# Performance work log

Hardware: AMD Instinct MI355X
Metric: run time of the kernel (lower is better)

Reference implementation:

```python
import jax, jax.numpy as jnp
import numpy as np

N_NODES = 100000
N_EDGES = 1600000
D = 128            # in_channels == hidden_channels
N_CLASSES = 10
N_GRAPHS = 512
N_CONVS = 3        # num_layers - 1


def _linear_params(key, d_in, d_out):
    kw, kb = jax.random.split(key)
    bound = 1.0 / np.sqrt(d_in)
    w = jax.random.uniform(kw, (d_in, d_out), jnp.float32, -bound, bound)
    b = jax.random.uniform(kb, (d_out,), jnp.float32, -bound, bound)
    return w, b


def setup_inputs() -> dict:
    key = jax.random.key(0)
    ks = jax.random.split(key, 16)
    x = jax.random.normal(ks[0], (N_NODES, D), jnp.float32)
    edge_index = jax.random.randint(ks[1], (2, N_EDGES), 0, N_NODES, jnp.int64)
    batch = jnp.sort(jax.random.randint(ks[2], (N_NODES,), 0, N_GRAPHS, jnp.int64))
    inp = {"x": x, "edge_index": edge_index, "batch": batch}
    # 3 GIN convs, each an MLP: Linear(D,D) -> ReLU -> Linear(D,D)
    for i in range(N_CONVS):
        w1, b1 = _linear_params(ks[3 + 2 * i], D, D)
        w2, b2 = _linear_params(ks[4 + 2 * i], D, D)
        inp[f"w1_{i}"], inp[f"b1_{i}"] = w1, b1
        inp[f"w2_{i}"], inp[f"b2_{i}"] = w2, b2
    wl, bl = _linear_params(ks[10], D, N_CLASSES)
    inp["w_lin"], inp["b_lin"] = wl, bl
    return inp


def _gin_conv(x, src, dst, w1, b1, w2, b2):
    # sum_{j->i} x_j  (scatter-add over edges), eps = 0 (PyG default)
    agg = jax.ops.segment_sum(x[src], dst, num_segments=N_NODES)
    h = agg + x  # (1 + eps) * x + aggregate
    h = jax.nn.relu(h @ w1 + b1) @ w2 + b2  # nn.Sequential MLP
    return h


def reference(x, edge_index, batch,
              w1_0, b1_0, w2_0, b2_0,
              w1_1, b1_1, w2_1, b2_1,
              w1_2, b1_2, w2_2, b2_2,
              w_lin, b_lin):
    src, dst = edge_index[0], edge_index[1]
    params = [(w1_0, b1_0, w2_0, b2_0),
              (w1_1, b1_1, w2_1, b2_1),
              (w1_2, b1_2, w2_2, b2_2)]
    for (w1, b1, w2, b2) in params:
        x = _gin_conv(x, src, dst, w1, b1, w2, b2)
        x = jax.nn.relu(x)
    pooled = jax.ops.segment_sum(x, batch, num_segments=N_GRAPHS)  # global_add_pool
    return pooled @ w_lin + b_lin
```

## Files before the change

kernel.cpp:

```cpp
#include <hip/hip_runtime.h>
#include <hip/hip_bf16.h>

#define N_NODES 100000
#define N_EDGES 1600000
#define DIM 128
#define N_GRAPHS 512
#define N_CLASSES 10
#define SCAN_CHUNK 1024

#define NBK 782
#define EB 8192
#define NEB 196
#define HN (NBK * NEB)
#define NCH_HIST ((HN + SCAN_CHUNK - 1) / SCAN_CHUNK)
#define NCH_CNT ((N_NODES + SCAN_CHUNK - 1) / SCAN_CHUNK)

#define POOL_CHUNK 128
#define NPB ((N_NODES + POOL_CHUNK - 1) / POOL_CHUNK)

typedef __attribute__((ext_vector_type(8))) short short8;
typedef __attribute__((ext_vector_type(4))) float floatx4;

__device__ __forceinline__ uint bfround(float f) {
    uint u = __builtin_bit_cast(uint, f);
    return (u + 0x7fffu + ((u >> 16) & 1u)) >> 16;
}
__device__ __forceinline__ float bflo(uint u) { return __builtin_bit_cast(float, u << 16); }
__device__ __forceinline__ float bfhi(uint u) { return __builtin_bit_cast(float, u & 0xffff0000u); }
__device__ __forceinline__ float bf2f(ushort u) { return __builtin_bit_cast(float, (uint)u << 16); }

__device__ __forceinline__ void addrow(float* a, uint4 v) {
    a[0] += bflo(v.x); a[1] += bfhi(v.x);
    a[2] += bflo(v.y); a[3] += bfhi(v.y);
    a[4] += bflo(v.z); a[5] += bfhi(v.z);
    a[6] += bflo(v.w); a[7] += bfhi(v.w);
}


__global__ void k_cvt_x(const float* __restrict__ x, ushort* __restrict__ xb, int n4) {
    int i = blockIdx.x * blockDim.x + threadIdx.x;
    int stride = gridDim.x * blockDim.x;
    for (; i < n4; i += stride) {
        floatx4 v = *(const floatx4*)(x + (size_t)i * 4);
        ushort4 o;
        o.x = (ushort)bfround(v.x);
        o.y = (ushort)bfround(v.y);
        o.z = (ushort)bfround(v.z);
        o.w = (ushort)bfround(v.w);
        *(ushort4*)(xb + (size_t)i * 4) = o;
    }
}

struct WPtrs { const float* w[6]; };

__global__ __launch_bounds__(256) void k_cvt_w(WPtrs wp, ushort* __restrict__ Wt) {
    int m = blockIdx.x >> 6;
    int idx = (blockIdx.x & 63) * 256 + threadIdx.x;
    int n = idx >> 7, k = idx & 127;
    Wt[(size_t)m * 16384 + idx] = (ushort)bfround(wp.w[m][k * 128 + n]);
}


__global__ void k_zero(int* __restrict__ p, int n) {
    int i = blockIdx.x * blockDim.x + threadIdx.x;
    int stride = gridDim.x * blockDim.x;
    for (; i < n; i += stride) p[i] = 0;
}

__global__ __launch_bounds__(256) void k_hist(const int* __restrict__ dstv,
                                              int* __restrict__ hist) {
    __shared__ int cnt[NBK];
    int blk = blockIdx.x, tid = threadIdx.x;
    for (int i = tid; i < NBK; i += 256) cnt[i] = 0;
    __syncthreads();
    int base = blk * EB;
    int end = min(base + EB, N_EDGES);
    for (int i = base + tid; i < end; i += 256) atomicAdd(&cnt[dstv[i] >> 7], 1);
    __syncthreads();
    for (int b = tid; b < NBK; b += 256) hist[b * NEB + blk] = cnt[b];
}

__global__ __launch_bounds__(256) void k_reduce(const int* __restrict__ src, int n,
                                                int* __restrict__ chunk_sums) {
    int base = blockIdx.x * SCAN_CHUNK;
    int tid = threadIdx.x;
    int s = 0;
    for (int i = tid; i < SCAN_CHUNK; i += 256) {
        int idx = base + i;
        if (idx < n) s += src[idx];
    }
    __shared__ int red[256];
    red[tid] = s;
    __syncthreads();
    for (int off = 128; off > 0; off >>= 1) {
        if (tid < off) red[tid] += red[tid + off];
        __syncthreads();
    }
    if (tid == 0) chunk_sums[blockIdx.x] = red[0];
}

__global__ __launch_bounds__(256) void k_scan_c(int* __restrict__ chunk_sums, int nch,
                                                int* __restrict__ total_out) {
    __shared__ int sm[256];
    int tid = threadIdx.x;
    int v = (tid < nch) ? chunk_sums[tid] : 0;
    sm[tid] = v;
    __syncthreads();
    for (int off = 1; off < 256; off <<= 1) {
        int t = (tid >= off) ? sm[tid - off] : 0;
        __syncthreads();
        sm[tid] += t;
        __syncthreads();
    }
    if (tid < nch) chunk_sums[tid] = sm[tid] - v;
    if (tid == 255) *total_out = sm[255];
}

__global__ __launch_bounds__(256) void k_apply(const int* __restrict__ src,
                                               const int* __restrict__ chunk_sums,
                                               int* __restrict__ dst, int n) {
    int base = blockIdx.x * SCAN_CHUNK;
    int tid = threadIdx.x;
    int i0 = base + tid * 4;
    int v[4];
    int s = 0;
    #pragma unroll
    for (int j = 0; j < 4; j++) {
        int idx = i0 + j;
        v[j] = (idx < n) ? src[idx] : 0;
        s += v[j];
    }
    __shared__ int sc[256];
    sc[tid] = s;
    __syncthreads();
    for (int off = 1; off < 256; off <<= 1) {
        int t = (tid >= off) ? sc[tid - off] : 0;
        __syncthreads();
        sc[tid] += t;
        __syncthreads();
    }
    int excl = sc[tid] - s + chunk_sums[blockIdx.x];
    #pragma unroll
    for (int j = 0; j < 4; j++) {
        int idx = i0 + j;
        if (idx < n) dst[idx] = excl;
        excl += v[j];
    }
}

__global__ __launch_bounds__(256) void k_scatter(const int* __restrict__ srcv,
                                                 const int* __restrict__ dstv,
                                                 const int* __restrict__ hists,
                                                 uint* __restrict__ sorted) {
    __shared__ int cur[NBK];
    int blk = blockIdx.x, tid = threadIdx.x;
    for (int b = tid; b < NBK; b += 256) cur[b] = hists[b * NEB + blk];
    __syncthreads();
    int base = blk * EB;
    int end = min(base + EB, N_EDGES);
    for (int i = base + tid; i < end; i += 256) {
        int s = srcv[i], d = dstv[i];
        int p = atomicAdd(&cur[d >> 7], 1);
        sorted[p] = (uint)s | ((uint)(d & 127) << 17);
    }
}

__global__ __launch_bounds__(256) void k_bcount_s(const int* __restrict__ hists,
                                                  const uint* __restrict__ sorted,
                                                  int* __restrict__ counts) {
    __shared__ int cnt[128];
    int b = blockIdx.x, tid = threadIdx.x;
    if (tid < 128) cnt[tid] = 0;
    __syncthreads();
    int s0 = hists[b * NEB];
    int s1 = (b == NBK - 1) ? N_EDGES : hists[(b + 1) * NEB];
    for (int i = s0 + tid; i < s1; i += 256) atomicAdd(&cnt[(sorted[i] >> 17) & 127], 1);
    __syncthreads();
    int node = (b << 7) + tid;
    if (tid < 128 && node < N_NODES) counts[node] = cnt[tid];
}

__global__ __launch_bounds__(256) void k_fill_s(const int* __restrict__ hists,
                                                const uint* __restrict__ sorted,
                                                const int* __restrict__ row_ptr,
                                                int* __restrict__ col) {
    __shared__ int cur[128];
    int b = blockIdx.x, tid = threadIdx.x;
    int node = (b << 7) + tid;
    if (tid < 128 && node < N_NODES) cur[tid] = row_ptr[node];
    __syncthreads();
    int s0 = hists[b * NEB];
    int s1 = (b == NBK - 1) ? N_EDGES : hists[(b + 1) * NEB];
    for (int i = s0 + tid; i < s1; i += 256) {
        uint e = sorted[i];
        int p = atomicAdd(&cur[(e >> 17) & 127], 1);
        col[p] = (int)(e & 0x1FFFFu);
    }
}

__global__ __launch_bounds__(256) void k_agg(const uint4* __restrict__ xr,
                                             const int* __restrict__ row_ptr,
                                             const int* __restrict__ col,
                                             uint4* __restrict__ hr) {
    int node = (blockIdx.x << 2) + (threadIdx.x >> 6);
    if (node >= N_NODES) return;
    int lane = threadIdx.x & 63;
    int grp = lane >> 4;
    int l16 = lane & 15;

    float acc[8];
    if (grp == 0) {
        uint4 sv = xr[(size_t)node * 16 + l16];
        acc[0] = bflo(sv.x); acc[1] = bfhi(sv.x);
        acc[2] = bflo(sv.y); acc[3] = bfhi(sv.y);
        acc[4] = bflo(sv.z); acc[5] = bfhi(sv.z);
        acc[6] = bflo(sv.w); acc[7] = bfhi(sv.w);
    } else {
        #pragma unroll
        for (int i = 0; i < 8; i++) acc[i] = 0.f;
    }

    int b = row_ptr[node], e = row_ptr[node + 1];
    for (int j0 = b; j0 < e; j0 += 64) {
        int rem = e - j0;
        int chunk = rem < 64 ? rem : 64;
        int myidx = (lane < chunk) ? col[j0 + lane] : 0;
        int iters = (chunk + 15) >> 4;
        for (int f = 0; f < iters; f++) {
            int p = (f << 4) + grp;
            int s0 = __shfl(myidx, (p      < chunk) ? p      : 0);
            int s1 = __shfl(myidx, (p + 4  < chunk) ? p + 4  : 0);
            int s2 = __shfl(myidx, (p + 8  < chunk) ? p + 8  : 0);
            int s3 = __shfl(myidx, (p + 12 < chunk) ? p + 12 : 0);
            uint4 v0 = xr[(size_t)s0 * 16 + l16];
            uint4 v1 = xr[(size_t)s1 * 16 + l16];
            uint4 v2 = xr[(size_t)s2 * 16 + l16];
            uint4 v3 = xr[(size_t)s3 * 16 + l16];
            if (p < chunk)      addrow(acc, v0);
            if (p + 4 < chunk)  addrow(acc, v1);
            if (p + 8 < chunk)  addrow(acc, v2);
            if (p + 12 < chunk) addrow(acc, v3);
        }
    }

    #pragma unroll
    for (int i = 0; i < 8; i++) {
        acc[i] += __shfl_xor(acc[i], 16);
        acc[i] += __shfl_xor(acc[i], 32);
    }

    if (grp == 0) {
        uint4 o;
        o.x = bfround(acc[0]) | (bfround(acc[1]) << 16);
        o.y = bfround(acc[2]) | (bfround(acc[3]) << 16);
        o.z = bfround(acc[4]) | (bfround(acc[5]) << 16);
        o.w = bfround(acc[6]) | (bfround(acc[7]) << 16);
        hr[(size_t)node * 16 + l16] = o;
    }
}

__device__ __forceinline__ int loff(int row, int byte) {
    return row * 256 + (byte ^ ((row & 7) << 4));
}

__global__ __launch_bounds__(256) void k_mlp(const ushort* __restrict__ hin,
                                             ushort* __restrict__ xout,
                                             const ushort* __restrict__ W1t,
                                             const float* __restrict__ b1,
                                             const ushort* __restrict__ W2t,
                                             const float* __restrict__ b2) {
    __shared__ alignas(16) char hT[64 * 256];
    __shared__ alignas(16) char tT[64 * 256];
    int tid = threadIdx.x;
    int lane = tid & 63;
    int wave = tid >> 6;
    int node0 = blockIdx.x * 64;
    int l15 = lane & 15;
    int lhi = lane >> 4;

    #pragma unroll
    for (int it = 0; it < 4; ++it) {
        int idx = it * 256 + tid;
        int row = idx >> 4;
        int cb = (idx & 15) * 16;
        int gn = node0 + row;
        floatx4 v = {0.f, 0.f, 0.f, 0.f};
        if (gn < N_NODES) v = *(const floatx4*)(hin + (size_t)gn * 128 + cb / 2);
        *(floatx4*)(hT + loff(row, cb)) = v;
    }
    __syncthreads();

    int ncol0 = wave * 32;
    short8 bf[4][2];
    #pragma unroll
    for (int ks = 0; ks < 4; ks++)
        #pragma unroll
        for (int nf = 0; nf < 2; nf++) {
            int nrow = ncol0 + nf * 16 + l15;
            bf[ks][nf] = *(const short8*)(W1t + nrow * 128 + ks * 32 + lhi * 8);
        }

    floatx4 acc[4][2];
    #pragma unroll
    for (int m = 0; m < 4; m++)
        #pragma unroll
        for (int nf = 0; nf < 2; nf++) {
            float bias = b1[ncol0 + nf * 16 + l15];
            acc[m][nf] = (floatx4){bias, bias, bias, bias};
        }

    #pragma unroll
    for (int ks = 0; ks < 4; ks++) {
        short8 af[4];
        #pragma unroll
        for (int m = 0; m < 4; m++)
            af[m] = *(const short8*)(hT + loff(m * 16 + l15, ks * 64 + lhi * 16));
        #pragma unroll
        for (int m = 0; m < 4; m++)
            #pragma unroll
            for (int nf = 0; nf < 2; nf++)
                acc[m][nf] = __builtin_amdgcn_mfma_f32_16x16x32_bf16(af[m], bf[ks][nf], acc[m][nf], 0, 0, 0);
    }
    #pragma unroll
    for (int m = 0; m < 4; m++)
        #pragma unroll
        for (int nf = 0; nf < 2; nf++) {
            int colb = (ncol0 + nf * 16 + l15) * 2;
            #pragma unroll
            for (int j = 0; j < 4; j++) {
                int row = m * 16 + lhi * 4 + j;
                float t = acc[m][nf][j];
                t = t > 0.f ? t : 0.f;
                *(ushort*)(tT + loff(row, colb)) = (ushort)bfround(t);
            }
        }
    __syncthreads();

    #pragma unroll
    for (int ks = 0; ks < 4; ks++)
        #pragma unroll
        for (int nf = 0; nf < 2; nf++) {
            int nrow = ncol0 + nf * 16 + l15;
            bf[ks][nf] = *(const short8*)(W2t + nrow * 128 + ks * 32 + lhi * 8);
        }
    #pragma unroll
    for (int m = 0; m < 4; m++)
        #pragma unroll
        for (int nf = 0; nf < 2; nf++) {
            float bias = b2[ncol0 + nf * 16 + l15];
            acc[m][nf] = (floatx4){bias, bias, bias, bias};
        }

    #pragma unroll
    for (int ks = 0; ks < 4; ks++) {
        short8 af[4];
        #pragma unroll
        for (int m = 0; m < 4; m++)
            af[m] = *(const short8*)(tT + loff(m * 16 + l15, ks * 64 + lhi * 16));
        #pragma unroll
        for (int m = 0; m < 4; m++)
            #pragma unroll
            for (int nf = 0; nf < 2; nf++)
                acc[m][nf] = __builtin_amdgcn_mfma_f32_16x16x32_bf16(af[m], bf[ks][nf], acc[m][nf], 0, 0, 0);
    }
    #pragma unroll
    for (int m = 0; m < 4; m++)
        #pragma unroll
        for (int nf = 0; nf < 2; nf++) {
            int colb = (ncol0 + nf * 16 + l15) * 2;
            #pragma unroll
            for (int j = 0; j < 4; j++) {
                int row = m * 16 + lhi * 4 + j;
                float t = acc[m][nf][j];
                t = t > 0.f ? t : 0.f;
                *(ushort*)(hT + loff(row, colb)) = (ushort)bfround(t);
            }
        }
    __syncthreads();
    #pragma unroll
    for (int it = 0; it < 4; ++it) {
        int idx = it * 256 + tid;
        int row = idx >> 4;
        int cb = (idx & 15) * 16;
        int gn = node0 + row;
        if (gn < N_NODES)
            *(floatx4*)(xout + (size_t)gn * 128 + cb / 2) = *(const floatx4*)(hT + loff(row, cb));
    }
}

__global__ __launch_bounds__(256) void k_pool(const uint* __restrict__ x,
                                              const int* __restrict__ batch,
                                              float* __restrict__ pooled) {
    int n0 = blockIdx.x * POOL_CHUNK;
    int wave = threadIdx.x >> 6;
    int lane = threadIdx.x & 63;
    float a0 = 0.f, a1 = 0.f;
    int cur = -1;
    int endn = min(n0 + POOL_CHUNK, N_NODES);
    for (int n = n0 + wave; n < endn; n += 4) {
        int g = batch[n];
        if (g != cur) {
            if (cur >= 0) {
                atomicAdd(&pooled[cur * 128 + lane * 2], a0);
                atomicAdd(&pooled[cur * 128 + lane * 2 + 1], a1);
            }
            cur = g; a0 = 0.f; a1 = 0.f;
        }
        uint v = x[(size_t)n * 64 + lane];
        a0 += bflo(v); a1 += bfhi(v);
    }
    if (cur >= 0) {
        atomicAdd(&pooled[cur * 128 + lane * 2], a0);
        atomicAdd(&pooled[cur * 128 + lane * 2 + 1], a1);
    }
}

__global__ __launch_bounds__(64) void k_final(const float* __restrict__ pooled,
                                              const float* __restrict__ wl,
                                              const float* __restrict__ bl,
                                              float* __restrict__ out) {
    int g = blockIdx.x;
    int o = threadIdx.x;
    if (o >= N_CLASSES) return;
    float acc = bl[o];
    for (int k = 0; k < 128; k++) acc += pooled[g * 128 + k] * wl[k * N_CLASSES + o];
    out[g * N_CLASSES + o] = acc;
}


extern "C" void kernel_launch(void* const* d_in, const int* in_sizes, int n_in,
                              void* d_out, int out_size, void* d_ws, size_t ws_size,
                              hipStream_t stream) {
    const float* x0  = (const float*)d_in[0];
    const int* ei    = (const int*)d_in[1];
    const int* batch = (const int*)d_in[2];
    const float* W1[3] = {(const float*)d_in[3], (const float*)d_in[7],  (const float*)d_in[11]};
    const float* B1[3] = {(const float*)d_in[4], (const float*)d_in[8],  (const float*)d_in[12]};
    const float* W2[3] = {(const float*)d_in[5], (const float*)d_in[9],  (const float*)d_in[13]};
    const float* B2[3] = {(const float*)d_in[6], (const float*)d_in[10], (const float*)d_in[14]};
    const float* wl = (const float*)d_in[15];
    const float* bl = (const float*)d_in[16];
    float* out = (float*)d_out;

    const int* srcv = ei;
    const int* dstv = ei + N_EDGES;

    char* w = (char*)d_ws;
    ushort* xb = (ushort*)w;
    ushort* hb = xb + (size_t)N_NODES * DIM;
    ushort* wt = hb + (size_t)N_NODES * DIM;
    float* pooled = (float*)(wt + 6 * 128 * 128);
    int* row_ptr = (int*)(pooled + N_GRAPHS * DIM);
    int* counts  = row_ptr + (N_NODES + 2);
    int* colidx  = counts + N_NODES;
    int* chunk_sums = colidx + N_EDGES;
    int* hist    = chunk_sums + 256;
    uint* sorted = (uint*)(hist + HN + 1);

    hipLaunchKernelGGL(k_cvt_x, dim3(2048), dim3(256), 0, stream, x0, xb, N_NODES * DIM / 4);
    WPtrs wp;
    wp.w[0] = W1[0]; wp.w[1] = W2[0]; wp.w[2] = W1[1];
    wp.w[3] = W2[1]; wp.w[4] = W1[2]; wp.w[5] = W2[2];
    hipLaunchKernelGGL(k_cvt_w, dim3(6 * 64), dim3(256), 0, stream, wp, wt);
    hipLaunchKernelGGL(k_zero, dim3(64), dim3(256), 0, stream, (int*)pooled, N_GRAPHS * DIM);

    hipLaunchKernelGGL(k_hist, dim3(NEB), dim3(256), 0, stream, dstv, hist);
    hipLaunchKernelGGL(k_reduce, dim3(NCH_HIST), dim3(256), 0, stream, hist, HN, chunk_sums);
    hipLaunchKernelGGL(k_scan_c, dim3(1), dim3(256), 0, stream, chunk_sums, NCH_HIST, hist + HN);
    hipLaunchKernelGGL(k_apply, dim3(NCH_HIST), dim3(256), 0, stream, hist, chunk_sums, hist, HN);
    hipLaunchKernelGGL(k_scatter, dim3(NEB), dim3(256), 0, stream, srcv, dstv, hist, sorted);
    hipLaunchKernelGGL(k_bcount_s, dim3(NBK), dim3(256), 0, stream, hist, sorted, counts);
    hipLaunchKernelGGL(k_reduce, dim3(NCH_CNT), dim3(256), 0, stream, counts, N_NODES, chunk_sums);
    hipLaunchKernelGGL(k_scan_c, dim3(1), dim3(256), 0, stream, chunk_sums, NCH_CNT, row_ptr + N_NODES);
    hipLaunchKernelGGL(k_apply, dim3(NCH_CNT), dim3(256), 0, stream, counts, chunk_sums, row_ptr, N_NODES);
    hipLaunchKernelGGL(k_fill_s, dim3(NBK), dim3(256), 0, stream, hist, sorted, row_ptr, colidx);

    dim3 aggGrid((N_NODES + 3) / 4), aggBlk(256);
    dim3 mlpGrid((N_NODES + 63) / 64), mlpBlk(256);
    for (int l = 0; l < 3; l++) {
        hipLaunchKernelGGL(k_agg, aggGrid, aggBlk, 0, stream,
                           (const uint4*)xb, row_ptr, colidx, (uint4*)hb);
        hipLaunchKernelGGL(k_mlp, mlpGrid, mlpBlk, 0, stream,
                           hb, xb, wt + (size_t)(2 * l) * 16384, B1[l],
                           wt + (size_t)(2 * l + 1) * 16384, B2[l]);
    }

    hipLaunchKernelGGL(k_pool, dim3(NPB), dim3(256), 0, stream, (const uint*)xb, batch, pooled);
    hipLaunchKernelGGL(k_final, dim3(N_GRAPHS), dim3(64), 0, stream, pooled, wl, bl, out);
}
```

Before: 346.3 us.

## Fuse neighbor aggregation into GIN MLP kernel with ping-pong buffers

Merges the separate aggregation and MLP kernels into one kernel. Each block gathers and sums neighbor rows for its 64-node tile straight into swizzled shared memory, then runs the MFMA MLP on that tile. Two ping-pong buffers replace the intermediate bf16 round trip through global memory. This removes one write and one read of the aggregated features per layer, plus one launch. The cost is that each wave now handles 16 nodes in sequence, which gives fewer independent waves to hide gather latency, raises register and LDS pressure per block, and adds load imbalance from skewed degrees.

Result: slower. 380.1 us (+9.7%).

```diff
diff --git a/kernel.cpp b/kernel.cpp
--- a/kernel.cpp
+++ b/kernel.cpp
@@ -18,6 +18,9 @@
 #define POOL_CHUNK 128
 #define NPB ((N_NODES + POOL_CHUNK - 1) / POOL_CHUNK)
 
+#define GIN_TILE 64
+#define NGB ((N_NODES + GIN_TILE - 1) / GIN_TILE)
+
 typedef __attribute__((ext_vector_type(8))) short short8;
 typedef __attribute__((ext_vector_type(4))) float floatx4;
 
@@ -27,7 +30,6 @@
 }
 __device__ __forceinline__ float bflo(uint u) { return __builtin_bit_cast(float, u << 16); }
 __device__ __forceinline__ float bfhi(uint u) { return __builtin_bit_cast(float, u & 0xffff0000u); }
-__device__ __forceinline__ float bf2f(ushort u) { return __builtin_bit_cast(float, (uint)u << 16); }
 
 __device__ __forceinline__ void addrow(float* a, uint4 v) {
     a[0] += bflo(v.x); a[1] += bfhi(v.x);
@@ -198,72 +200,13 @@
     }
 }
 
-__global__ __launch_bounds__(256) void k_agg(const uint4* __restrict__ xr,
+__device__ __forceinline__ int loff(int row, int byte) {
+    return row * 256 + (byte ^ ((row & 7) << 4));
+}
+
+__global__ __launch_bounds__(256) void k_gin(const uint4* __restrict__ xr,
                                              const int* __restrict__ row_ptr,
                                              const int* __restrict__ col,
-                                             uint4* __restrict__ hr) {
-    int node = (blockIdx.x << 2) + (threadIdx.x >> 6);
-    if (node >= N_NODES) return;
-    int lane = threadIdx.x & 63;
-    int grp = lane >> 4;
-    int l16 = lane & 15;
-
-    float acc[8];
-    if (grp == 0) {
-        uint4 sv = xr[(size_t)node * 16 + l16];
-        acc[0] = bflo(sv.x); acc[1] = bfhi(sv.x);
-        acc[2] = bflo(sv.y); acc[3] = bfhi(sv.y);
-        acc[4] = bflo(sv.z); acc[5] = bfhi(sv.z);
-        acc[6] = bflo(sv.w); acc[7] = bfhi(sv.w);
-    } else {
-        #pragma unroll
-        for (int i = 0; i < 8; i++) acc[i] = 0.f;
-    }
-
-    int b = row_ptr[node], e = row_ptr[node + 1];
-    for (int j0 = b; j0 < e; j0 += 64) {
-        int rem = e - j0;
-        int chunk = rem < 64 ? rem : 64;
-        int myidx = (lane < chunk) ? col[j0 + lane] : 0;
-        int iters = (chunk + 15) >> 4;
-        for (int f = 0; f < iters; f++) {
-            int p = (f << 4) + grp;
-            int s0 = __shfl(myidx, (p      < chunk) ? p      : 0);
-            int s1 = __shfl(myidx, (p + 4  < chunk) ? p + 4  : 0);
-            int s2 = __shfl(myidx, (p + 8  < chunk) ? p + 8  : 0);
-            int s3 = __shfl(myidx, (p + 12 < chunk) ? p + 12 : 0);
-            uint4 v0 = xr[(size_t)s0 * 16 + l16];
-            uint4 v1 = xr[(size_t)s1 * 16 + l16];
-            uint4 v2 = xr[(size_t)s2 * 16 + l16];
-            uint4 v3 = xr[(size_t)s3 * 16 + l16];
-            if (p < chunk)      addrow(acc, v0);
-            if (p + 4 < chunk)  addrow(acc, v1);
-            if (p + 8 < chunk)  addrow(acc, v2);
-            if (p + 12 < chunk) addrow(acc, v3);
-        }
-    }
-
-    #pragma unroll
-    for (int i = 0; i < 8; i++) {
-        acc[i] += __shfl_xor(acc[i], 16);
-        acc[i] += __shfl_xor(acc[i], 32);
-    }
-
-    if (grp == 0) {
-        uint4 o;
-        o.x = bfround(acc[0]) | (bfround(acc[1]) << 16);
-        o.y = bfround(acc[2]) | (bfround(acc[3]) << 16);
-        o.z = bfround(acc[4]) | (bfround(acc[5]) << 16);
-        o.w = bfround(acc[6]) | (bfround(acc[7]) << 16);
-        hr[(size_t)node * 16 + l16] = o;
-    }
-}
-
-__device__ __forceinline__ int loff(int row, int byte) {
-    return row * 256 + (byte ^ ((row & 7) << 4));
-}
-
-__global__ __launch_bounds__(256) void k_mlp(const ushort* __restrict__ hin,
                                              ushort* __restrict__ xout,
                                              const ushort* __restrict__ W1t,
                                              const float* __restrict__ b1,
@@ -274,22 +217,71 @@
     int tid = threadIdx.x;
     int lane = tid & 63;
     int wave = tid >> 6;
-    int node0 = blockIdx.x * 64;
+    int node0 = blockIdx.x * GIN_TILE;
+    int grp = lane >> 4;
+    int l16 = lane & 15;
+
+    for (int i = 0; i < 16; i++) {
+        int row = wave * 16 + i;
+        int node = node0 + row;
+        if (node >= N_NODES) {
+            if (grp == 0) *(uint4*)(hT + loff(row, l16 * 16)) = make_uint4(0, 0, 0, 0);
+            continue;
+        }
+        float acc[8];
+        if (grp == 0) {
+            uint4 sv = xr[(size_t)node * 16 + l16];
+            acc[0] = bflo(sv.x); acc[1] = bfhi(sv.x);
+            acc[2] = bflo(sv.y); acc[3] = bfhi(sv.y);
+            acc[4] = bflo(sv.z); acc[5] = bfhi(sv.z);
+            acc[6] = bflo(sv.w); acc[7] = bfhi(sv.w);
+        } else {
+            #pragma unroll
+            for (int q = 0; q < 8; q++) acc[q] = 0.f;
+        }
+
+        int b = row_ptr[node], e = row_ptr[node + 1];
+        for (int j0 = b; j0 < e; j0 += 64) {
+            int rem = e - j0;
+            int chunk = rem < 64 ? rem : 64;
+            int myidx = (lane < chunk) ? col[j0 + lane] : 0;
+            int iters = (chunk + 15) >> 4;
+            for (int f = 0; f < iters; f++) {
+                int p = (f << 4) + grp;
+                int s0 = __shfl(myidx, (p      < chunk) ? p      : 0);
+                int s1 = __shfl(myidx, (p + 4  < chunk) ? p + 4  : 0);
+                int s2 = __shfl(myidx, (p + 8  < chunk) ? p + 8  : 0);
+                int s3 = __shfl(myidx, (p + 12 < chunk) ? p + 12 : 0);
+                uint4 v0 = xr[(size_t)s0 * 16 + l16];
+                uint4 v1 = xr[(size_t)s1 * 16 + l16];
+                uint4 v2 = xr[(size_t)s2 * 16 + l16];
+                uint4 v3 = xr[(size_t)s3 * 16 + l16];
+                if (p < chunk)      addrow(acc, v0);
+                if (p + 4 < chunk)  addrow(acc, v1);
+                if (p + 8 < chunk)  addrow(acc, v2);
+                if (p + 12 < chunk) addrow(acc, v3);
+            }
+        }
+
+        #pragma unroll
+        for (int q = 0; q < 8; q++) {
+            acc[q] += __shfl_xor(acc[q], 16);
+            acc[q] += __shfl_xor(acc[q], 32);
+        }
+
+        if (grp == 0) {
+            uint4 o;
+            o.x = bfround(acc[0]) | (bfround(acc[1]) << 16);
+            o.y = bfround(acc[2]) | (bfround(acc[3]) << 16);
+            o.z = bfround(acc[4]) | (bfround(acc[5]) << 16);
+            o.w = bfround(acc[6]) | (bfround(acc[7]) << 16);
+            *(uint4*)(hT + loff(row, l16 * 16)) = o;
+        }
+    }
+    __syncthreads();
+
     int l15 = lane & 15;
     int lhi = lane >> 4;
-
-    #pragma unroll
-    for (int it = 0; it < 4; ++it) {
-        int idx = it * 256 + tid;
-        int row = idx >> 4;
-        int cb = (idx & 15) * 16;
-        int gn = node0 + row;
-        floatx4 v = {0.f, 0.f, 0.f, 0.f};
-        if (gn < N_NODES) v = *(const floatx4*)(hin + (size_t)gn * 128 + cb / 2);
-        *(floatx4*)(hT + loff(row, cb)) = v;
-    }
-    __syncthreads();
-
     int ncol0 = wave * 32;
     short8 bf[4][2];
     #pragma unroll
@@ -475,16 +467,17 @@
     hipLaunchKernelGGL(k_apply, dim3(NCH_CNT), dim3(256), 0, stream, counts, chunk_sums, row_ptr, N_NODES);
     hipLaunchKernelGGL(k_fill_s, dim3(NBK), dim3(256), 0, stream, hist, sorted, row_ptr, colidx);
 
-    dim3 aggGrid((N_NODES + 3) / 4), aggBlk(256);
-    dim3 mlpGrid((N_NODES + 63) / 64), mlpBlk(256);
+    dim3 ginGrid(NGB), ginBlk(256);
+    const ushort* xin = xb;
+    ushort* xo = hb;
     for (int l = 0; l < 3; l++) {
-        hipLaunchKernelGGL(k_agg, aggGrid, aggBlk, 0, stream,
-                           (const uint4*)xb, row_ptr, colidx, (uint4*)hb);
-        hipLaunchKernelGGL(k_mlp, mlpGrid, mlpBlk, 0, stream,
-                           hb, xb, wt + (size_t)(2 * l) * 16384, B1[l],
+        hipLaunchKernelGGL(k_gin, ginGrid, ginBlk, 0, stream,
+                           (const uint4*)xin, row_ptr, colidx, xo,
+                           wt + (size_t)(2 * l) * 16384, B1[l],
                            wt + (size_t)(2 * l + 1) * 16384, B2[l]);
-    }
-
-    hipLaunchKernelGGL(k_pool, dim3(NPB), dim3(256), 0, stream, (const uint*)xb, batch, pooled);
+        const ushort* t = xin; xin = xo; xo = (ushort*)t;
+    }
+
+    hipLaunchKernelGGL(k_pool, dim3(NPB), dim3(256), 0, stream, (const uint*)hb, batch, pooled);
     hipLaunchKernelGGL(k_final, dim3(N_GRAPHS), dim3(64), 0, stream, pooled, wl, bl, out);
 }
```
